# Optimization experiments

Hardware: AMD Instinct MI355X
Metric: run time of the kernel (lower is better)

## Reference

```python
import jax, jax.numpy as jnp
import numpy as np

B, N, D_IN, H, MSG, L, TGT, N_LAYERS = 8, 1024, 64, 128, 128, 5, 12, 3


def setup_inputs() -> dict:
    key = jax.random.key(0)
    ks = jax.random.split(key, 10)
    g = jax.random.uniform(ks[0], (B, N, N), jnp.float32)          # adjacency / edge weights
    h_in = jax.random.uniform(ks[1], (B, N, D_IN), jnp.float32)    # node features (positive -> all nodes present)
    e = jax.random.randint(ks[2], (B, N, N), 0, L).astype(jnp.int32)  # discrete edge labels in [0, L)

    def init(k, shape, fan):
        return jax.random.normal(k, shape, jnp.float32) / np.sqrt(fan)

    A = init(ks[3], (L, H, MSG), H)            # per-edge-label message matrices
    Wi = init(ks[4], (MSG, 3 * H), MSG)        # GRU input weights (r,z,n)
    Wh = init(ks[5], (H, 3 * H), H)            # GRU hidden weights (r,z,n)
    bi = jnp.zeros((3 * H,), jnp.float32)
    bh = jnp.zeros((3 * H,), jnp.float32)
    W_gate = init(ks[6], (2 * H, TGT), 2 * H)  # readout gating net i([h_T, h_0])
    b_gate = jnp.zeros((TGT,), jnp.float32)
    W_out = init(ks[7], (H, TGT), H)           # readout net j(h_T)
    b_out = jnp.zeros((TGT,), jnp.float32)
    return dict(g=g, h_in=h_in, e=e, A=A, Wi=Wi, Wh=Wh, bi=bi, bh=bh,
                W_gate=W_gate, b_gate=b_gate, W_out=W_out, b_out=b_out)


def _gru_step(m, h, Wi, Wh, bi, bh):
    # Single GRU step applied independently per node: m [B,N,MSG], h [B,N,H]
    gi = m @ Wi + bi
    gh = h @ Wh + bh
    i_r, i_z, i_n = jnp.split(gi, 3, axis=-1)
    h_r, h_z, h_n = jnp.split(gh, 3, axis=-1)
    r = jax.nn.sigmoid(i_r + h_r)
    z = jax.nn.sigmoid(i_z + h_z)
    n = jnp.tanh(i_n + r * h_n)
    return (1.0 - z) * n + z * h


def reference(g, h_in, e, A, Wi, Wh, bi, bh, W_gate, b_gate, W_out, b_out):
    n_labels, hidden = A.shape[0], A.shape[1]
    # pad input features with zeros up to hidden_state_size
    h0 = jnp.pad(h_in, ((0, 0), (0, 0), (0, hidden - h_in.shape[-1])))
    # node-presence mask: sum(|h_in|) > 0  -> [B,N,1]
    node_mask = (jnp.sum(jnp.abs(h_in), axis=-1, keepdims=True) > 0).astype(h0.dtype)
    h = h0
    for _ in range(N_LAYERS):  # weight-tied message passing
        # per-label candidate messages: M_l[b,w,:] = h[b,w,:] @ A_l  -> [L,B,N,MSG]
        Ml = jnp.einsum('bwd,ldo->lbwo', h, A)
        agg = jnp.zeros(h.shape[:2] + (A.shape[2],), h.dtype)
        for l in range(n_labels):
            # mask by adjacency AND matching edge label, sum over neighbors w
            w_l = g * (e == l).astype(g.dtype)                  # [B,N,N]
            agg = agg + jnp.einsum('bvw,bwo->bvo', w_l, Ml[l])  # [B,N,MSG]
        h = _gru_step(agg, h, Wi, Wh, bi, bh) * node_mask
    hT = h
    # GGNN readout: sum_v sigmoid(i([h_T, h_0])) * j(h_T), masked on present nodes
    gate = jax.nn.sigmoid(jnp.concatenate([hT, h0], axis=-1) @ W_gate + b_gate)
    out = gate * (hT @ W_out + b_out)                            # [B,N,TGT]
    read_mask = (jnp.sum(h0, axis=-1, keepdims=True) > 0).astype(h0.dtype)
    return jnp.sum(out * read_mask, axis=1)                      # [B,TGT]
```

## Files before the change

### kernel.cpp

```cpp
#include <hip/hip_runtime.h>

#define B_      8
#define N_      1024
#define DIN_    64
#define H_      128
#define MSG2    128
#define L_      5
#define TGT_    12
#define NLAYERS_ 3
#define CAT_    640
#define NODES   (B_ * N_)
#define KSPLIT  3

typedef __attribute__((ext_vector_type(8))) short s16x8;
typedef __attribute__((ext_vector_type(4))) float f32x4;

#define GLD16(G, L) __builtin_amdgcn_global_load_lds( \
    (const __attribute__((address_space(1))) void*)(G), \
    (__attribute__((address_space(3))) void*)(L), 16, 0, 0)

__device__ __forceinline__ float sigmoidf_(float x) { return 1.f / (1.f + __expf(-x)); }

__device__ __forceinline__ unsigned short f2bf(float x) {
  unsigned int u = __float_as_uint(x);
  u += 0x7FFFu + ((u >> 16) & 1u);
  return (unsigned short)(u >> 16);
}
__device__ __forceinline__ float bf2f(unsigned short u) {
  return __uint_as_float(((unsigned int)u) << 16);
}

__global__ __launch_bounds__(256) void k_init(const float* __restrict__ h_in,
                                              float* __restrict__ h,
                                              float* __restrict__ h0,
                                              unsigned short* __restrict__ X,
                                              float* __restrict__ maskA,
                                              float* __restrict__ maskR) {
  int node = blockIdx.x * 4 + (threadIdx.x >> 6);
  int lane = threadIdx.x & 63;
  float v = h_in[(size_t)node * DIN_ + lane];
  size_t base = (size_t)node * H_;
  h[base + lane] = v;   h[base + 64 + lane] = 0.f;
  h0[base + lane] = v;  h0[base + 64 + lane] = 0.f;
  unsigned short hi = f2bf(v);
  unsigned short lo = f2bf(v - bf2f(hi));
  size_t xb = (size_t)node * 256;
  X[xb + lane] = hi;        X[xb + 64 + lane] = 0;
  X[xb + 128 + lane] = lo;  X[xb + 192 + lane] = 0;
  float sa = fabsf(v), ss = v;
  for (int off = 32; off > 0; off >>= 1) {
    sa += __shfl_down(sa, off);
    ss += __shfl_down(ss, off);
  }
  if (lane == 0) {
    maskA[node] = (sa > 0.f) ? 1.f : 0.f;
    maskR[node] = (ss > 0.f) ? 1.f : 0.f;
  }
}

__global__ __launch_bounds__(256) void k_pack(const float* __restrict__ g,
                                              const int* __restrict__ e,
                                              unsigned short* __restrict__ Gb,
                                              unsigned char* __restrict__ Eb) {
  size_t i8 = ((size_t)blockIdx.x * 256 + threadIdx.x) * 8;
  float4 g0 = *(const float4*)&g[i8];
  float4 g1 = *(const float4*)&g[i8 + 4];
  int4   e0 = *(const int4*)&e[i8];
  int4   e1 = *(const int4*)&e[i8 + 4];
  ushort4 ga, gb;
  ga.x = f2bf(g0.x); ga.y = f2bf(g0.y); ga.z = f2bf(g0.z); ga.w = f2bf(g0.w);
  gb.x = f2bf(g1.x); gb.y = f2bf(g1.y); gb.z = f2bf(g1.z); gb.w = f2bf(g1.w);
  *(ushort4*)&Gb[i8]     = ga;
  *(ushort4*)&Gb[i8 + 4] = gb;
  uint2 ev;
  ev.x = (unsigned)(e0.x & 0xFF) | ((unsigned)(e0.y & 0xFF) << 8) |
         ((unsigned)(e0.z & 0xFF) << 16) | ((unsigned)(e0.w & 0xFF) << 24);
  ev.y = (unsigned)(e1.x & 0xFF) | ((unsigned)(e1.y & 0xFF) << 8) |
         ((unsigned)(e1.z & 0xFF) << 16) | ((unsigned)(e1.w & 0xFF) << 24);
  *(uint2*)&Eb[i8] = ev;
}

__global__ __launch_bounds__(256) void k_aprep(const float* __restrict__ A,
                                               unsigned short* __restrict__ ATh,
                                               unsigned short* __restrict__ ATl) {
  int idx = blockIdx.x * 256 + threadIdx.x;
  if (idx >= CAT_ * 128) return;
  int c = idx >> 7, d = idx & 127;
  int l = c >> 7, o = c & 127;
  float v = A[((size_t)l * 128 + d) * 128 + o];
  unsigned short hi = f2bf(v);
  ATh[idx] = hi;
  ATl[idx] = f2bf(v - bf2f(hi));
}

__global__ __launch_bounds__(256) void k_wprep(const float* __restrict__ Wi,
                                               const float* __restrict__ Wh,
                                               unsigned short* __restrict__ WiTh,
                                               unsigned short* __restrict__ WiTl,
                                               unsigned short* __restrict__ WhTh,
                                               unsigned short* __restrict__ WhTl) {
  int idx = blockIdx.x * 256 + threadIdx.x;
  if (idx < 384 * 128) {
    int c = idx >> 7, k = idx & 127;
    float v = Wi[(size_t)k * 384 + c];
    unsigned short hi = f2bf(v);
    WiTh[idx] = hi; WiTl[idx] = f2bf(v - bf2f(hi));
  } else if (idx < 2 * 384 * 128) {
    int i = idx - 384 * 128;
    int c = i >> 7, k = i & 127;
    float v = Wh[(size_t)k * 384 + c];
    unsigned short hi = f2bf(v);
    WhTh[i] = hi; WhTl[i] = f2bf(v - bf2f(hi));
  }
}

__global__ __launch_bounds__(256) void k_gemmT(const unsigned short* __restrict__ X,
                                               const unsigned short* __restrict__ ATh,
                                               const unsigned short* __restrict__ ATl,
                                               unsigned short* __restrict__ McatT) {
  __shared__ __align__(16) unsigned short Ah[64 * 40];
  __shared__ __align__(16) unsigned short Al[64 * 40];
  __shared__ __align__(16) unsigned short Bh[128 * 40];
  __shared__ __align__(16) unsigned short Bl2[128 * 40];
  const int tid = threadIdx.x;
  const int c0 = blockIdx.x * 128;
  const int node0 = blockIdx.y * 64;
  const int b = node0 >> 10;
  const int w0 = node0 & 1023;
  const int wid = tid >> 6, lane = tid & 63;
  const int wr = wid >> 1, wc = wid & 1;
  const int lr = lane & 15, lg = lane >> 4;
  const int ar = tid >> 2, aq = (tid & 3) * 8;
  const int br = tid >> 1, bq = (tid & 1) * 16;
  f32x4 acc[2][4];
  #pragma unroll
  for (int m = 0; m < 2; ++m)
    #pragma unroll
    for (int n = 0; n < 4; ++n) acc[m][n] = {0.f, 0.f, 0.f, 0.f};
  for (int kk = 0; kk < 4; ++kk) {
    const int kb = kk * 32;
    *(uint4*)&Ah[ar * 40 + aq] = *(const uint4*)&X[(size_t)(node0 + ar) * 256 + kb + aq];
    *(uint4*)&Al[ar * 40 + aq] = *(const uint4*)&X[(size_t)(node0 + ar) * 256 + 128 + kb + aq];
    const unsigned short* bh = ATh + (size_t)(c0 + br) * 128 + kb + bq;
    const unsigned short* bl = ATl + (size_t)(c0 + br) * 128 + kb + bq;
    *(uint4*)&Bh[br * 40 + bq]      = *(const uint4*)bh;
    *(uint4*)&Bh[br * 40 + bq + 8]  = *(const uint4*)(bh + 8);
    *(uint4*)&Bl2[br * 40 + bq]     = *(const uint4*)bl;
    *(uint4*)&Bl2[br * 40 + bq + 8] = *(const uint4*)(bl + 8);
    __syncthreads();
    s16x8 ah[2], al[2], bhf[4], blf[4];
    #pragma unroll
    for (int m = 0; m < 2; ++m) {
      int row = (wr * 32 + m * 16 + lr) * 40 + lg * 8;
      ah[m] = *(const s16x8*)&Ah[row];
      al[m] = *(const s16x8*)&Al[row];
    }
    #pragma unroll
    for (int n = 0; n < 4; ++n) {
      int row = (wc * 64 + n * 16 + lr) * 40 + lg * 8;
      bhf[n] = *(const s16x8*)&Bh[row];
      blf[n] = *(const s16x8*)&Bl2[row];
    }
    #pragma unroll
    for (int m = 0; m < 2; ++m)
      #pragma unroll
      for (int n = 0; n < 4; ++n) {
        acc[m][n] = __builtin_amdgcn_mfma_f32_16x16x32_bf16(ah[m], bhf[n], acc[m][n], 0, 0, 0);
        acc[m][n] = __builtin_amdgcn_mfma_f32_16x16x32_bf16(ah[m], blf[n], acc[m][n], 0, 0, 0);
        acc[m][n] = __builtin_amdgcn_mfma_f32_16x16x32_bf16(al[m], bhf[n], acc[m][n], 0, 0, 0);
      }
    __syncthreads();
  }
  #pragma unroll
  for (int m = 0; m < 2; ++m)
    #pragma unroll
    for (int n = 0; n < 4; ++n) {
      int c = c0 + wc * 64 + n * 16 + lr;
      int l = c >> 7, o = c & 127;
      int w = w0 + wr * 32 + m * 16 + lg * 4;
      ushort4 v;
      v.x = f2bf(acc[m][n][0]); v.y = f2bf(acc[m][n][1]);
      v.z = f2bf(acc[m][n][2]); v.w = f2bf(acc[m][n][3]);
      *(ushort4*)&McatT[(((size_t)b * L_ + l) * MSG2 + o) * N_ + w] = v;
    }
}

__global__ __launch_bounds__(256, 3) void k_agg_mfma(const unsigned short* __restrict__ Gb,
                                                     const unsigned char* __restrict__ Eb,
                                                     const unsigned short* __restrict__ McatT,
                                                     float* __restrict__ aggP) {
  __shared__ __align__(16) unsigned short GtS[2][64 * 32];
  __shared__ __align__(16) unsigned char  EtS[2][64 * 40];
  __shared__ __align__(16) unsigned short BlS[2][L_][64 * 32];
  char* GtB = (char*)GtS;
  char* EtB = (char*)EtS;
  char* BlB = (char*)BlS;

  const int tid = threadIdx.x;
  const int fid = blockIdx.x;
  const int xcd = fid & 7;
  const int s   = fid >> 3;
  const int p   = xcd * 3 + (s >> 5);
  const int idx = s & 31;
  const int v0  = (idx & 15) * 64;
  const int oh  = idx >> 4;
  const int ks  = p >> 3;
  const int b   = p & 7;

  const int wid  = tid >> 6, lane = tid & 63;
  const int wr   = wid >> 1, wc = wid & 1;
  const int lr   = lane & 15, lg = lane >> 4;

  f32x4 acc[2][2];
  #pragma unroll
  for (int m = 0; m < 2; ++m)
    #pragma unroll
    for (int n = 0; n < 2; ++n) acc[m][n] = {0.f, 0.f, 0.f, 0.f};

  const int ar = tid >> 2, aq = (tid & 3) * 8;
  const int rsrc = ar ^ ((ar >> 2) & 1);
  const int kq   = aq ^ ((rsrc & 3) << 3);
  const size_t garow  = ((size_t)b * N_ + v0 + ar) * N_;
  const size_t garowS = ((size_t)b * N_ + v0 + rsrc) * N_;
  const size_t mrowS  = (((size_t)b * L_) * MSG2 + oh * 64 + rsrc) * N_;
  const size_t lstep  = (size_t)MSG2 * N_;
  const int ksbase = ks * 352;
  const int ntile  = (ks == 2) ? 10 : 11;

  const int ldst = tid * 16;
  const int et_w = ar * 40 + aq;
  const int fsw  = (lr & 7) << 4;

  {
    const int kb = ksbase;
    GLD16(Gb + garowS + kb + kq, GtB + ldst);
    #pragma unroll
    for (int l = 0; l < L_; ++l)
      GLD16(McatT + mrowS + (size_t)l * lstep + kb + kq, BlB + l * 4096 + ldst);
    uint2 ev0 = *(const uint2*)&Eb[garow + kb + aq];
    *(uint2*)(EtB + et_w) = ev0;
  }
  __syncthreads();

  for (int kk = 0; kk < ntile; ++kk) {
    const int cur = kk & 1;
    const int nxt = cur ^ 1;
    uint2 ev;
    if (kk + 1 < ntile) {
      const int kb = ksbase + (kk + 1) * 32;
      GLD16(Gb + garowS + kb + kq, GtB + nxt * 4096 + ldst);
      #pragma unroll
      for (int l = 0; l < L_; ++l)
        GLD16(McatT + mrowS + (size_t)l * lstep + kb + kq,
              BlB + nxt * 20480 + l * 4096 + ldst);
      ev = *(const uint2*)&Eb[garow + kb + aq];
    }

    {
      const char* Gc = GtB + cur * 4096;
      const char* Ec = EtB + cur * 2560;
      const char* Bc = BlB + cur * 20480;
      s16x8 gt[2]; uint2 et[2];
      #pragma unroll
      for (int m = 0; m < 2; ++m) {
        int row = wr * 32 + m * 16 + lr;
        gt[m] = *(const s16x8*)(Gc + ((row * 64 + lg * 16) ^ fsw));
        et[m] = *(const uint2*)(Ec + row * 40 + lg * 8);
      }
      #pragma unroll
      for (int l = 0; l < L_; ++l) {
        s16x8 bfr[2];
        #pragma unroll
        for (int n = 0; n < 2; ++n) {
          int row = wc * 32 + n * 16 + lr;
          bfr[n] = *(const s16x8*)(Bc + l * 4096 + ((row * 64 + lg * 16) ^ fsw));
        }
        #pragma unroll
        for (int m = 0; m < 2; ++m) {
          unsigned int w0e = et[m].x, w1e = et[m].y;
          s16x8 af;
          af[0] = (((w0e      ) & 0xFFu) == (unsigned)l) ? gt[m][0] : (short)0;
          af[1] = (((w0e >>  8) & 0xFFu) == (unsigned)l) ? gt[m][1] : (short)0;
          af[2] = (((w0e >> 16) & 0xFFu) == (unsigned)l) ? gt[m][2] : (short)0;
          af[3] = (((w0e >> 24) & 0xFFu) == (unsigned)l) ? gt[m][3] : (short)0;
          af[4] = (((w1e      ) & 0xFFu) == (unsigned)l) ? gt[m][4] : (short)0;
          af[5] = (((w1e >>  8) & 0xFFu) == (unsigned)l) ? gt[m][5] : (short)0;
          af[6] = (((w1e >> 16) & 0xFFu) == (unsigned)l) ? gt[m][6] : (short)0;
          af[7] = (((w1e >> 24) & 0xFFu) == (unsigned)l) ? gt[m][7] : (short)0;
          #pragma unroll
          for (int n = 0; n < 2; ++n)
            acc[m][n] = __builtin_amdgcn_mfma_f32_16x16x32_bf16(af, bfr[n], acc[m][n], 0, 0, 0);
        }
      }
    }

    if (kk + 1 < ntile) *(uint2*)(EtB + nxt * 2560 + et_w) = ev;
    __syncthreads();
  }

  float* op = aggP + ((size_t)ks * NODES + (size_t)b * N_ + v0) * MSG2 + oh * 64;
  #pragma unroll
  for (int m = 0; m < 2; ++m)
    #pragma unroll
    for (int n = 0; n < 2; ++n)
      #pragma unroll
      for (int j = 0; j < 4; ++j) {
        int row = wr * 32 + m * 16 + lg * 4 + j;
        int col = wc * 32 + n * 16 + lr;
        op[(size_t)row * MSG2 + col] = acc[m][n][j];
      }
}

__global__ __launch_bounds__(256) void k_xprep(const float* __restrict__ aggP,
                                               unsigned short* __restrict__ Xm) {
  const size_t slab = (size_t)NODES * MSG2;
  size_t i4 = ((size_t)blockIdx.x * 256 + threadIdx.x) * 4;
  float4 s;
  s.x = 0.f; s.y = 0.f; s.z = 0.f; s.w = 0.f;
  #pragma unroll
  for (int k = 0; k < KSPLIT; ++k) {
    float4 v = *(const float4*)&aggP[k * slab + i4];
    s.x += v.x; s.y += v.y; s.z += v.z; s.w += v.w;
  }
  size_t node = i4 >> 7;
  size_t j = i4 & 127;
  ushort4 hi, lo;
  hi.x = f2bf(s.x); lo.x = f2bf(s.x - bf2f(hi.x));
  hi.y = f2bf(s.y); lo.y = f2bf(s.y - bf2f(hi.y));
  hi.z = f2bf(s.z); lo.z = f2bf(s.z - bf2f(hi.z));
  hi.w = f2bf(s.w); lo.w = f2bf(s.w - bf2f(hi.w));
  *(ushort4*)&Xm[node * 256 + j]       = hi;
  *(ushort4*)&Xm[node * 256 + 128 + j] = lo;
}

__global__ __launch_bounds__(256) void k_gates_mfma(const unsigned short* __restrict__ Xm,
                                                    const unsigned short* __restrict__ Xh,
                                                    const unsigned short* __restrict__ WiTh,
                                                    const unsigned short* __restrict__ WiTl,
                                                    const unsigned short* __restrict__ WhTh,
                                                    const unsigned short* __restrict__ WhTl,
                                                    float* __restrict__ gates) {
  __shared__ __align__(16) unsigned short Ah[64 * 40];
  __shared__ __align__(16) unsigned short Al[64 * 40];
  __shared__ __align__(16) unsigned short Bh[128 * 40];
  __shared__ __align__(16) unsigned short Bl2[128 * 40];
  const int tid = threadIdx.x;
  const int z = blockIdx.z;
  const unsigned short* Xp  = z ? Xh : Xm;
  const unsigned short* WTh = z ? WhTh : WiTh;
  const unsigned short* WTl = z ? WhTl : WiTl;
  const int c0 = blockIdx.x * 128;
  const int node0 = blockIdx.y * 64;
  const int wid = tid >> 6, lane = tid & 63;
  const int wr = wid >> 1, wc = wid & 1;
  const int lr = lane & 15, lg = lane >> 4;
  const int ar = tid >> 2, aq = (tid & 3) * 8;
  const int br = tid >> 1, bq = (tid & 1) * 16;
  f32x4 acc[2][4];
  #pragma unroll
  for (int m = 0; m < 2; ++m)
    #pragma unroll
    for (int n = 0; n < 4; ++n) acc[m][n] = {0.f, 0.f, 0.f, 0.f};
  for (int kk = 0; kk < 4; ++kk) {
    const int kb = kk * 32;
    *(uint4*)&Ah[ar * 40 + aq] = *(const uint4*)&Xp[(size_t)(node0 + ar) * 256 + kb + aq];
    *(uint4*)&Al[ar * 40 + aq] = *(const uint4*)&Xp[(size_t)(node0 + ar) * 256 + 128 + kb + aq];
    const unsigned short* bh = WTh + (size_t)(c0 + br) * 128 + kb + bq;
    const unsigned short* bl = WTl + (size_t)(c0 + br) * 128 + kb + bq;
    *(uint4*)&Bh[br * 40 + bq]      = *(const uint4*)bh;
    *(uint4*)&Bh[br * 40 + bq + 8]  = *(const uint4*)(bh + 8);
    *(uint4*)&Bl2[br * 40 + bq]     = *(const uint4*)bl;
    *(uint4*)&Bl2[br * 40 + bq + 8] = *(const uint4*)(bl + 8);
    __syncthreads();
    s16x8 ah[2], al[2], bhf[4], blf[4];
    #pragma unroll
    for (int m = 0; m < 2; ++m) {
      int row = (wr * 32 + m * 16 + lr) * 40 + lg * 8;
      ah[m] = *(const s16x8*)&Ah[row];
      al[m] = *(const s16x8*)&Al[row];
    }
    #pragma unroll
    for (int n = 0; n < 4; ++n) {
      int row = (wc * 64 + n * 16 + lr) * 40 + lg * 8;
      bhf[n] = *(const s16x8*)&Bh[row];
      blf[n] = *(const s16x8*)&Bl2[row];
    }
    #pragma unroll
    for (int m = 0; m < 2; ++m)
      #pragma unroll
      for (int n = 0; n < 4; ++n) {
        acc[m][n] = __builtin_amdgcn_mfma_f32_16x16x32_bf16(ah[m], bhf[n], acc[m][n], 0, 0, 0);
        acc[m][n] = __builtin_amdgcn_mfma_f32_16x16x32_bf16(ah[m], blf[n], acc[m][n], 0, 0, 0);
        acc[m][n] = __builtin_amdgcn_mfma_f32_16x16x32_bf16(al[m], bhf[n], acc[m][n], 0, 0, 0);
      }
    __syncthreads();
  }
  #pragma unroll
  for (int m = 0; m < 2; ++m)
    #pragma unroll
    for (int n = 0; n < 4; ++n) {
      int c = c0 + wc * 64 + n * 16 + lr;
      int row = node0 + wr * 32 + m * 16 + lg * 4;
      #pragma unroll
      for (int j = 0; j < 4; ++j)
        gates[(size_t)(row + j) * 768 + z * 384 + c] = acc[m][n][j];
    }
}

__global__ __launch_bounds__(256) void k_gru_elt(const float* __restrict__ gates,
                                                 const float* __restrict__ bi,
                                                 const float* __restrict__ bh,
                                                 const float* __restrict__ maskA,
                                                 float* __restrict__ h,
                                                 unsigned short* __restrict__ X) {
  const int t = threadIdx.x;
  const int node = blockIdx.x * 8 + (t >> 5);
  const int j4 = (t & 31) * 4;
  const size_t gb = (size_t)node * 768;
  float4 gir = *(const float4*)&gates[gb + j4];
  float4 giz = *(const float4*)&gates[gb + 128 + j4];
  float4 gin = *(const float4*)&gates[gb + 256 + j4];
  float4 ghr = *(const float4*)&gates[gb + 384 + j4];
  float4 ghz = *(const float4*)&gates[gb + 512 + j4];
  float4 ghn = *(const float4*)&gates[gb + 640 + j4];
  float4 bir = *(const float4*)&bi[j4];
  float4 biz = *(const float4*)&bi[128 + j4];
  float4 bin = *(const float4*)&bi[256 + j4];
  float4 bhr = *(const float4*)&bh[j4];
  float4 bhz = *(const float4*)&bh[128 + j4];
  float4 bhn = *(const float4*)&bh[256 + j4];
  float4 hv = *(const float4*)&h[(size_t)node * 128 + j4];
  float m = maskA[node];
  float4 ho;
  {
    float r = sigmoidf_(gir.x + bir.x + ghr.x + bhr.x);
    float z = sigmoidf_(giz.x + biz.x + ghz.x + bhz.x);
    float nn = tanhf(gin.x + bin.x + r * (ghn.x + bhn.x));
    ho.x = ((1.f - z) * nn + z * hv.x) * m;
  }
  {
    float r = sigmoidf_(gir.y + bir.y + ghr.y + bhr.y);
    float z = sigmoidf_(giz.y + biz.y + ghz.y + bhz.y);
    float nn = tanhf(gin.y + bin.y + r * (ghn.y + bhn.y));
    ho.y = ((1.f - z) * nn + z * hv.y) * m;
  }
  {
    float r = sigmoidf_(gir.z + bir.z + ghr.z + bhr.z);
    float z = sigmoidf_(giz.z + biz.z + ghz.z + bhz.z);
    float nn = tanhf(gin.z + bin.z + r * (ghn.z + bhn.z));
    ho.z = ((1.f - z) * nn + z * hv.z) * m;
  }
  {
    float r = sigmoidf_(gir.w + bir.w + ghr.w + bhr.w);
    float z = sigmoidf_(giz.w + biz.w + ghz.w + bhz.w);
    float nn = tanhf(gin.w + bin.w + r * (ghn.w + bhn.w));
    ho.w = ((1.f - z) * nn + z * hv.w) * m;
  }
  *(float4*)&h[(size_t)node * 128 + j4] = ho;
  ushort4 hi, lo;
  hi.x = f2bf(ho.x); lo.x = f2bf(ho.x - bf2f(hi.x));
  hi.y = f2bf(ho.y); lo.y = f2bf(ho.y - bf2f(hi.y));
  hi.z = f2bf(ho.z); lo.z = f2bf(ho.z - bf2f(hi.z));
  hi.w = f2bf(ho.w); lo.w = f2bf(ho.w - bf2f(hi.w));
  *(ushort4*)&X[(size_t)node * 256 + j4]       = hi;
  *(ushort4*)&X[(size_t)node * 256 + 128 + j4] = lo;
}

__global__ __launch_bounds__(256) void k_readP(const float* __restrict__ h,
                                               const float* __restrict__ h0,
                                               const float* __restrict__ Wg,
                                               const float* __restrict__ Wo,
                                               float* __restrict__ PT) {
  __shared__ float Xt[64][65];
  __shared__ float Wt[64][25];
  const int tid = threadIdx.x;
  const int node0 = blockIdx.x * 64;
  const int row = tid >> 2;
  const int cg  = tid & 3;
  float acc[6] = {0.f, 0.f, 0.f, 0.f, 0.f, 0.f};
  const int sr = tid >> 2;
  const int sk = (tid & 3) * 16;
  #pragma unroll
  for (int kb = 0; kb < 4; ++kb) {
    const float* src = (kb < 2 ? h : h0) + (size_t)(node0 + sr) * 128 + (kb & 1) * 64 + sk;
    #pragma unroll
    for (int q = 0; q < 4; ++q)
      *(float4*)&Xt[sr][sk + q * 4] = *(const float4*)(src + q * 4);
    #pragma unroll
    for (int j = 0; j < 6; ++j) {
      int idx = tid * 6 + j;
      int rk = idx / 24;
      int c24 = idx - rk * 24;
      int gk = kb * 64 + rk;
      float wv;
      if (c24 < 12) wv = Wg[(size_t)gk * TGT_ + c24];
      else          wv = (gk < 128) ? Wo[(size_t)gk * TGT_ + (c24 - 12)] : 0.f;
      Wt[rk][c24] = wv;
    }
    __syncthreads();
    #pragma unroll 8
    for (int k = 0; k < 64; ++k) {
      float x = Xt[row][k];
      #pragma unroll
      for (int j = 0; j < 6; ++j)
        acc[j] += x * Wt[k][cg * 6 + j];
    }
    __syncthreads();
  }
  #pragma unroll
  for (int j = 0; j < 6; ++j)
    PT[(size_t)(cg * 6 + j) * NODES + node0 + row] = acc[j];
}

__global__ __launch_bounds__(256) void k_readR(const float* __restrict__ PT,
                                               const float* __restrict__ maskR,
                                               const float* __restrict__ bg,
                                               const float* __restrict__ bo,
                                               float* __restrict__ out) {
  __shared__ float red[256];
  const int tid = threadIdx.x;
  const int b = blockIdx.x / TGT_;
  const int t = blockIdx.x - b * TGT_;
  const float bgt = bg[t], bot = bo[t];
  float s = 0.f;
  #pragma unroll
  for (int i = 0; i < 4; ++i) {
    int node = b * N_ + i * 256 + tid;
    float p1 = PT[(size_t)t * NODES + node] + bgt;
    float p2 = PT[(size_t)(12 + t) * NODES + node] + bot;
    s += sigmoidf_(p1) * p2 * maskR[node];
  }
  red[tid] = s;
  __syncthreads();
  #pragma unroll
  for (int off = 128; off > 0; off >>= 1) {
    if (tid < off) red[tid] += red[tid + off];
    __syncthreads();
  }
  if (tid == 0) out[b * TGT_ + t] = red[0];
}

extern "C" void kernel_launch(void* const* d_in, const int* in_sizes, int n_in,
                              void* d_out, int out_size, void* d_ws, size_t ws_size,
                              hipStream_t stream) {
  (void)in_sizes; (void)n_in; (void)out_size; (void)ws_size;
  const float* g    = (const float*)d_in[0];
  const float* h_in = (const float*)d_in[1];
  const int*   e    = (const int*)d_in[2];
  const float* A    = (const float*)d_in[3];
  const float* Wi   = (const float*)d_in[4];
  const float* Wh   = (const float*)d_in[5];
  const float* bi   = (const float*)d_in[6];
  const float* bh   = (const float*)d_in[7];
  const float* Wg   = (const float*)d_in[8];
  const float* bg   = (const float*)d_in[9];
  const float* Wo   = (const float*)d_in[10];
  const float* bo   = (const float*)d_in[11];
  float* out = (float*)d_out;
  float* ws  = (float*)d_ws;

  float* h     = ws;
  float* h0    = h + (size_t)NODES * H_;
  float* maskA = h0 + (size_t)NODES * H_;
  float* maskR = maskA + NODES;
  unsigned short* X    = (unsigned short*)(maskR + NODES);
  unsigned short* Xm   = X + (size_t)NODES * 256;
  unsigned short* ATh  = Xm + (size_t)NODES * 256;
  unsigned short* ATl  = ATh + CAT_ * 128;
  unsigned short* WiTh = ATl + CAT_ * 128;
  unsigned short* WiTl = WiTh + 384 * 128;
  unsigned short* WhTh = WiTl + 384 * 128;
  unsigned short* WhTl = WhTh + 384 * 128;
  unsigned short* Gb   = WhTl + 384 * 128;
  unsigned char*  Eb   = (unsigned char*)(Gb + (size_t)NODES * N_);
  float* aggP = (float*)(Eb + (size_t)NODES * N_);
  unsigned short* McatT = (unsigned short*)(aggP + (size_t)KSPLIT * NODES * MSG2);
  float* gates = aggP;
  float* PT = (float*)Xm;

  k_init<<<NODES / 4, 256, 0, stream>>>(h_in, h, h0, X, maskA, maskR);
  k_pack<<<(NODES * N_ / 8) / 256, 256, 0, stream>>>(g, e, Gb, Eb);
  k_aprep<<<(CAT_ * 128 + 255) / 256, 256, 0, stream>>>(A, ATh, ATl);
  k_wprep<<<(2 * 384 * 128 + 255) / 256, 256, 0, stream>>>(Wi, Wh, WiTh, WiTl, WhTh, WhTl);
  for (int layer = 0; layer < NLAYERS_; ++layer) {
    k_gemmT<<<dim3(CAT_ / 128, NODES / 64), 256, 0, stream>>>(X, ATh, ATl, McatT);
    k_agg_mfma<<<(N_ / 64) * 2 * KSPLIT * B_, 256, 0, stream>>>(Gb, Eb, McatT, aggP);
    k_xprep<<<(NODES * MSG2 / 4) / 256, 256, 0, stream>>>(aggP, Xm);
    k_gates_mfma<<<dim3(384 / 128, NODES / 64, 2), 256, 0, stream>>>(Xm, X, WiTh, WiTl, WhTh, WhTl, gates);
    k_gru_elt<<<NODES / 8, 256, 0, stream>>>(gates, bi, bh, maskA, h, X);
  }
  k_readP<<<NODES / 64, 256, 0, stream>>>(h, h0, Wg, Wo, PT);
  k_readR<<<B_ * TGT_, 256, 0, stream>>>(PT, maskR, bg, bo, out);
}
```

Before: 257.7 us.

## Triple-buffer aggregation K-loop with manual vmcnt waits and fewer K splits

Reworks the label-masked aggregation MFMA kernel to use a 3-stage LDS ring for the adjacency and message tiles. Loads are issued two tiles ahead, with explicit s_waitcnt vmcnt and a raw s_barrier replacing __syncthreads. It also cuts the K-split from 3 to 2, so each block handles 16 uniform tiles, the grid is smaller, and fewer partial sums go to the xprep reduction. The larger LDS footprint lowers occupancy to 2 blocks per CU. The hand-counted vmcnt(7) depends on the exact number of outstanding loads, which is fragile.

```diff
diff --git a/kernel.cpp b/kernel.cpp
--- a/kernel.cpp
+++ b/kernel.cpp
@@ -10,7 +10,8 @@
 #define NLAYERS_ 3
 #define CAT_    640
 #define NODES   (B_ * N_)
-#define KSPLIT  3
+#define KSPLIT  2
+#define NT_     16
 
 typedef __attribute__((ext_vector_type(8))) short s16x8;
 typedef __attribute__((ext_vector_type(4))) float f32x4;
@@ -185,22 +186,22 @@
     }
 }
 
-__global__ __launch_bounds__(256, 3) void k_agg_mfma(const unsigned short* __restrict__ Gb,
+__global__ __launch_bounds__(256, 2) void k_agg_mfma(const unsigned short* __restrict__ Gb,
                                                      const unsigned char* __restrict__ Eb,
                                                      const unsigned short* __restrict__ McatT,
                                                      float* __restrict__ aggP) {
-  __shared__ __align__(16) unsigned short GtS[2][64 * 32];
+  __shared__ __align__(16) unsigned short GtS[3][64 * 32];
+  __shared__ __align__(16) unsigned short BlS[3][L_][64 * 32];
   __shared__ __align__(16) unsigned char  EtS[2][64 * 40];
-  __shared__ __align__(16) unsigned short BlS[2][L_][64 * 32];
   char* GtB = (char*)GtS;
+  char* BlB = (char*)BlS;
   char* EtB = (char*)EtS;
-  char* BlB = (char*)BlS;
 
   const int tid = threadIdx.x;
   const int fid = blockIdx.x;
   const int xcd = fid & 7;
   const int s   = fid >> 3;
-  const int p   = xcd * 3 + (s >> 5);
+  const int p   = xcd * 2 + (s >> 5);
   const int idx = s & 31;
   const int v0  = (idx & 15) * 64;
   const int oh  = idx >> 4;
@@ -224,79 +225,83 @@
   const size_t garowS = ((size_t)b * N_ + v0 + rsrc) * N_;
   const size_t mrowS  = (((size_t)b * L_) * MSG2 + oh * 64 + rsrc) * N_;
   const size_t lstep  = (size_t)MSG2 * N_;
-  const int ksbase = ks * 352;
-  const int ntile  = (ks == 2) ? 10 : 11;
+  const int ksbase = ks * 512;
 
   const int ldst = tid * 16;
   const int et_w = ar * 40 + aq;
   const int fsw  = (lr & 7) << 4;
 
-  {
-    const int kb = ksbase;
-    GLD16(Gb + garowS + kb + kq, GtB + ldst);
-    #pragma unroll
-    for (int l = 0; l < L_; ++l)
-      GLD16(McatT + mrowS + (size_t)l * lstep + kb + kq, BlB + l * 4096 + ldst);
-    uint2 ev0 = *(const uint2*)&Eb[garow + kb + aq];
-    *(uint2*)(EtB + et_w) = ev0;
-  }
-  __syncthreads();
-
-  for (int kk = 0; kk < ntile; ++kk) {
-    const int cur = kk & 1;
-    const int nxt = cur ^ 1;
-    uint2 ev;
-    if (kk + 1 < ntile) {
-      const int kb = ksbase + (kk + 1) * 32;
-      GLD16(Gb + garowS + kb + kq, GtB + nxt * 4096 + ldst);
-      #pragma unroll
-      for (int l = 0; l < L_; ++l)
-        GLD16(McatT + mrowS + (size_t)l * lstep + kb + kq,
-              BlB + nxt * 20480 + l * 4096 + ldst);
-      ev = *(const uint2*)&Eb[garow + kb + aq];
-    }
-
-    {
-      const char* Gc = GtB + cur * 4096;
-      const char* Ec = EtB + cur * 2560;
-      const char* Bc = BlB + cur * 20480;
-      s16x8 gt[2]; uint2 et[2];
-      #pragma unroll
-      for (int m = 0; m < 2; ++m) {
-        int row = wr * 32 + m * 16 + lr;
-        gt[m] = *(const s16x8*)(Gc + ((row * 64 + lg * 16) ^ fsw));
-        et[m] = *(const uint2*)(Ec + row * 40 + lg * 8);
-      }
-      #pragma unroll
-      for (int l = 0; l < L_; ++l) {
-        s16x8 bfr[2];
-        #pragma unroll
-        for (int n = 0; n < 2; ++n) {
-          int row = wc * 32 + n * 16 + lr;
-          bfr[n] = *(const s16x8*)(Bc + l * 4096 + ((row * 64 + lg * 16) ^ fsw));
-        }
-        #pragma unroll
-        for (int m = 0; m < 2; ++m) {
-          unsigned int w0e = et[m].x, w1e = et[m].y;
-          s16x8 af;
-          af[0] = (((w0e      ) & 0xFFu) == (unsigned)l) ? gt[m][0] : (short)0;
-          af[1] = (((w0e >>  8) & 0xFFu) == (unsigned)l) ? gt[m][1] : (short)0;
-          af[2] = (((w0e >> 16) & 0xFFu) == (unsigned)l) ? gt[m][2] : (short)0;
-          af[3] = (((w0e >> 24) & 0xFFu) == (unsigned)l) ? gt[m][3] : (short)0;
-          af[4] = (((w1e      ) & 0xFFu) == (unsigned)l) ? gt[m][4] : (short)0;
-          af[5] = (((w1e >>  8) & 0xFFu) == (unsigned)l) ? gt[m][5] : (short)0;
-          af[6] = (((w1e >> 16) & 0xFFu) == (unsigned)l) ? gt[m][6] : (short)0;
-          af[7] = (((w1e >> 24) & 0xFFu) == (unsigned)l) ? gt[m][7] : (short)0;
-          #pragma unroll
-          for (int n = 0; n < 2; ++n)
-            acc[m][n] = __builtin_amdgcn_mfma_f32_16x16x32_bf16(af, bfr[n], acc[m][n], 0, 0, 0);
-        }
-      }
-    }
-
-    if (kk + 1 < ntile) *(uint2*)(EtB + nxt * 2560 + et_w) = ev;
-    __syncthreads();
-  }
+#define ISSUE(T) { \
+    const int kb_ = ksbase + (T) * 32; \
+    const int nb_ = (T) % 3; \
+    GLD16(Gb + garowS + kb_ + kq, GtB + nb_ * 4096 + ldst); \
+    _Pragma("unroll") \
+    for (int l_ = 0; l_ < L_; ++l_) \
+      GLD16(McatT + mrowS + (size_t)l_ * lstep + kb_ + kq, \
+            BlB + nb_ * 20480 + l_ * 4096 + ldst); }
+
+#define COMPUTE(T) { \
+    const char* Gc = GtB + ((T) % 3) * 4096; \
+    const char* Bc = BlB + ((T) % 3) * 20480; \
+    const char* Ec = EtB + ((T) & 1) * 2560; \
+    s16x8 gt[2]; uint2 et[2]; \
+    _Pragma("unroll") \
+    for (int m = 0; m < 2; ++m) { \
+      int row_ = wr * 32 + m * 16 + lr; \
+      gt[m] = *(const s16x8*)(Gc + ((row_ * 64 + lg * 16) ^ fsw)); \
+      et[m] = *(const uint2*)(Ec + row_ * 40 + lg * 8); \
+    } \
+    _Pragma("unroll") \
+    for (int l_ = 0; l_ < L_; ++l_) { \
+      s16x8 bfr[2]; \
+      _Pragma("unroll") \
+      for (int n = 0; n < 2; ++n) { \
+        int row_ = wc * 32 + n * 16 + lr; \
+        bfr[n] = *(const s16x8*)(Bc + l_ * 4096 + ((row_ * 64 + lg * 16) ^ fsw)); \
+      } \
+      _Pragma("unroll") \
+      for (int m = 0; m < 2; ++m) { \
+        unsigned int w0e = et[m].x, w1e = et[m].y; \
+        s16x8 af; \
+        af[0] = (((w0e      ) & 0xFFu) == (unsigned)l_) ? gt[m][0] : (short)0; \
+        af[1] = (((w0e >>  8) & 0xFFu) == (unsigned)l_) ? gt[m][1] : (short)0; \
+        af[2] = (((w0e >> 16) & 0xFFu) == (unsigned)l_) ? gt[m][2] : (short)0; \
+        af[3] = (((w0e >> 24) & 0xFFu) == (unsigned)l_) ? gt[m][3] : (short)0; \
+        af[4] = (((w1e      ) & 0xFFu) == (unsigned)l_) ? gt[m][4] : (short)0; \
+        af[5] = (((w1e >>  8) & 0xFFu) == (unsigned)l_) ? gt[m][5] : (short)0; \
+        af[6] = (((w1e >> 16) & 0xFFu) == (unsigned)l_) ? gt[m][6] : (short)0; \
+        af[7] = (((w1e >> 24) & 0xFFu) == (unsigned)l_) ? gt[m][7] : (short)0; \
+        _Pragma("unroll") \
+        for (int n = 0; n < 2; ++n) \
+          acc[m][n] = __builtin_amdgcn_mfma_f32_16x16x32_bf16(af, bfr[n], acc[m][n], 0, 0, 0); \
+      } \
+    } }
+
+#define STEP(T, EV) { \
+    if ((T) + 1 < NT_) asm volatile("s_waitcnt vmcnt(7)" ::: "memory"); \
+    else               asm volatile("s_waitcnt vmcnt(0)" ::: "memory"); \
+    *(uint2*)(EtB + ((T) & 1) * 2560 + et_w) = EV; \
+    asm volatile("s_waitcnt lgkmcnt(0)" ::: "memory"); \
+    __builtin_amdgcn_s_barrier(); \
+    if ((T) + 2 < NT_) { \
+      ISSUE((T) + 2); \
+      EV = *(const uint2*)&Eb[garow + ksbase + ((T) + 2) * 32 + aq]; \
+    } \
+    COMPUTE(T); }
+
+  uint2 evA, evB;
+  ISSUE(0);
+  evA = *(const uint2*)&Eb[garow + ksbase + aq];
+  ISSUE(1);
+  evB = *(const uint2*)&Eb[garow + ksbase + 32 + aq];
+
+  for (int t2 = 0; t2 < NT_; t2 += 2) {
+    STEP(t2, evA);
+    STEP(t2 + 1, evB);
+  }
+#undef ISSUE
+#undef COMPUTE
+#undef STEP
 
   float* op = aggP + ((size_t)ks * NODES + (size_t)b * N_ + v0) * MSG2 + oh * 64;
   #pragma unroll
```

New measurement: 239.9 us. 6.9% less time.
